# Kernel tuning notes

Measured on AMD Instinct MI355X. Metric: run time of the kernel, lower is better.

## Reference

```python
import jax, jax.numpy as jnp
import numpy as np

B, L, E, H = 2, 2048, 512, 8
D = E // H  # head_dim = 64


def setup_inputs() -> dict:
    key = jax.random.key(0)
    ks = jax.random.split(key, 12)
    s = 0.02
    return {
        "values": jax.random.normal(ks[0], (B, L, E), jnp.float32),
        "keys": jax.random.normal(ks[1], (B, L, E), jnp.float32),
        "query": jax.random.normal(ks[2], (B, L, E), jnp.float32),
        "mask": jax.random.randint(ks[3], (B, 1, L, L), 0, 2, jnp.int32),
        "Wv": jax.random.normal(ks[4], (E, E), jnp.float32) * s,
        "bv": jax.random.normal(ks[5], (E,), jnp.float32) * s,
        "Wk": jax.random.normal(ks[6], (E, E), jnp.float32) * s,
        "bk": jax.random.normal(ks[7], (E,), jnp.float32) * s,
        "Wq": jax.random.normal(ks[8], (E, E), jnp.float32) * s,
        "bq": jax.random.normal(ks[9], (E,), jnp.float32) * s,
        "Wo": jax.random.normal(ks[10], (E, E), jnp.float32) * s,
        "bo": jax.random.normal(ks[11], (E,), jnp.float32) * s,
    }


def reference(values, keys, query, mask, Wv, bv, Wk, bk, Wq, bq, Wo, bo):
    b, lq = query.shape[0], query.shape[1]
    # torch Linear: y = x @ W.T + b
    v = (values @ Wv.T + bv).reshape(b, -1, H, D)
    k = (keys @ Wk.T + bk).reshape(b, -1, H, D)
    q = (query @ Wq.T + bq).reshape(b, lq, H, D)
    energy = jnp.einsum("bqhd,bkhd->bhqk", q, k)  # [B,H,Lq,Lk]
    # mask applied BEFORE the scale, as in the original
    energy = jnp.where(mask == 0, jnp.float32(-1e20), energy)
    # NOTE: scales by sqrt(embed_size), not sqrt(head_dim) (faithful)
    attn = jax.nn.softmax(energy / jnp.sqrt(jnp.float32(E)), axis=3)
    out = jnp.einsum("bhql,blhd->bqhd", attn, v).reshape(b, lq, E)
    return out @ Wo.T + bo
```

## Files before the change

kernel.cpp:

```cpp
#include <hip/hip_runtime.h>
#include <hip/hip_bf16.h>
#include <math.h>

#define BB 2
#define LL 2048
#define EE 512
#define HH 8
#define DD 64
#define MM (BB * LL)
#define LW (LL / 64)

typedef short bf16x8 __attribute__((ext_vector_type(8)));
typedef float f32x4 __attribute__((ext_vector_type(4)));

#define MFMA16(a, b, c) __builtin_amdgcn_mfma_f32_16x16x32_bf16((a), (b), (c), 0, 0, 0)

__device__ __forceinline__ uint4 cvt8_bf16(const float4 a, const float4 b) {
    union { __hip_bfloat16 h[8]; uint4 u; } t;
    t.h[0] = __float2bfloat16(a.x); t.h[1] = __float2bfloat16(a.y);
    t.h[2] = __float2bfloat16(a.z); t.h[3] = __float2bfloat16(a.w);
    t.h[4] = __float2bfloat16(b.x); t.h[5] = __float2bfloat16(b.y);
    t.h[6] = __float2bfloat16(b.z); t.h[7] = __float2bfloat16(b.w);
    return t.u;
}

struct PrepArgs {
    const float* xsrc[3];
    __hip_bfloat16* xdst[3];
    const float* wsrc[4];
    __hip_bfloat16* wdst[4];
    const int* mask;
    unsigned long long* mbits;
};

__global__ __launch_bounds__(256) void prep(PrepArgs a) {
    const int blk = blockIdx.x;
    if (blk < 3072) {
        const int t = blk >> 10;
        const int i = ((blk & 1023) * 256 + threadIdx.x) * 8;
        const float* s = a.xsrc[t] + i;
        float4 f0 = *(const float4*)(s);
        float4 f1 = *(const float4*)(s + 4);
        *(uint4*)(a.xdst[t] + i) = cvt8_bf16(f0, f1);
    } else if (blk < 3584) {
        const int r = blk - 3072;
        const int t = r >> 7;
        const int i = ((r & 127) * 256 + threadIdx.x) * 8;
        const float* s = a.wsrc[t] + i;
        float4 f0 = *(const float4*)(s);
        float4 f1 = *(const float4*)(s + 4);
        *(uint4*)(a.wdst[t] + i) = cvt8_bf16(f0, f1);
    } else {
        const size_t idx = (size_t)(blk - 3584) * 256 + threadIdx.x;
        const int m = a.mask[idx];
        const unsigned long long w = __ballot(m != 0);
        if ((threadIdx.x & 63) == 0) a.mbits[idx >> 6] = w;
    }
}

__global__ __launch_bounds__(256) void transpose_v(
    const __hip_bfloat16* __restrict__ vb, __hip_bfloat16* __restrict__ vt) {
    __shared__ __hip_bfloat16 T[64][72];
    const int tid = threadIdx.x;
    const int l0 = blockIdx.x * 64;
    const int h = blockIdx.y;
    const int b = blockIdx.z;
    const int row = tid >> 2;
    const int cg = (tid & 3) * 16;

    const __hip_bfloat16* src = vb + ((size_t)b * LL + l0 + row) * EE + h * DD + cg;
    *(uint4*)&T[row][cg] = *(const uint4*)src;
    *(uint4*)&T[row][cg + 8] = *(const uint4*)(src + 8);
    __syncthreads();

    __hip_bfloat16 t[16];
    #pragma unroll
    for (int e = 0; e < 16; ++e) t[e] = T[cg + e][row];
    __hip_bfloat16* dst = vt + (((size_t)b * HH + h) * DD + row) * LL + l0 + cg;
    *(uint4*)&dst[0] = *(uint4*)&t[0];
    *(uint4*)&dst[8] = *(uint4*)&t[8];
}

struct QKVArgs {
    const __hip_bfloat16* X[3];
    const __hip_bfloat16* W[3];
    const float* bias[3];
    __hip_bfloat16* O[3];
};

__global__ __launch_bounds__(256) void gemm_qkv(QKVArgs p) {
    __shared__ __hip_bfloat16 Xs[128][72];
    __shared__ __hip_bfloat16 Ws[64][72];

    const int z = blockIdx.z;
    const __hip_bfloat16* __restrict__ X = p.X[z];
    const __hip_bfloat16* __restrict__ W = p.W[z];
    const float* __restrict__ bias = p.bias[z];
    __hip_bfloat16* __restrict__ O = p.O[z];
    const float oscale = (z == 0) ? 0.04419417382415922f : 1.0f;

    const int tid = threadIdx.x;
    const int wave = tid >> 6, lane = tid & 63;
    const int l15 = lane & 15, quad = lane >> 4;
    const int wm = wave * 32;
    const int m0 = blockIdx.y * 128, n0 = blockIdx.x * 64;

    const int arow = tid >> 1, acg = (tid & 1) * 32;
    const int brow = tid >> 2, bcg = (tid & 3) * 16;

    const __hip_bfloat16* Ag = X + (size_t)(m0 + arow) * EE + acg;
    const __hip_bfloat16* Bg = W + (size_t)(n0 + brow) * EE + bcg;

    f32x4 acc[2][4] = {};

    uint4 a0 = *(const uint4*)(Ag + 0),  a1 = *(const uint4*)(Ag + 8);
    uint4 a2 = *(const uint4*)(Ag + 16), a3 = *(const uint4*)(Ag + 24);
    uint4 b0 = *(const uint4*)(Bg + 0),  b1 = *(const uint4*)(Bg + 8);

    for (int k0 = 0; k0 < EE; k0 += 64) {
        *(uint4*)&Xs[arow][acg + 0]  = a0;
        *(uint4*)&Xs[arow][acg + 8]  = a1;
        *(uint4*)&Xs[arow][acg + 16] = a2;
        *(uint4*)&Xs[arow][acg + 24] = a3;
        *(uint4*)&Ws[brow][bcg + 0] = b0;
        *(uint4*)&Ws[brow][bcg + 8] = b1;
        __syncthreads();

        if (k0 + 64 < EE) {
            const __hip_bfloat16* an = Ag + k0 + 64;
            const __hip_bfloat16* bn = Bg + k0 + 64;
            a0 = *(const uint4*)(an + 0);  a1 = *(const uint4*)(an + 8);
            a2 = *(const uint4*)(an + 16); a3 = *(const uint4*)(an + 24);
            b0 = *(const uint4*)(bn + 0);  b1 = *(const uint4*)(bn + 8);
        }

        #pragma unroll
        for (int c = 0; c < 2; ++c) {
            bf16x8 af[2], bfr[4];
            #pragma unroll
            for (int i = 0; i < 2; ++i)
                af[i] = *(const bf16x8*)&Xs[wm + i * 16 + l15][c * 32 + quad * 8];
            #pragma unroll
            for (int j = 0; j < 4; ++j)
                bfr[j] = *(const bf16x8*)&Ws[j * 16 + l15][c * 32 + quad * 8];
            #pragma unroll
            for (int i = 0; i < 2; ++i)
                #pragma unroll
                for (int j = 0; j < 4; ++j)
                    acc[i][j] = MFMA16(af[i], bfr[j], acc[i][j]);
        }
        __syncthreads();
    }

    #pragma unroll
    for (int i = 0; i < 2; ++i)
        #pragma unroll
        for (int j = 0; j < 4; ++j) {
            const int n = n0 + j * 16 + l15;
            const float bv = bias[n];
            #pragma unroll
            for (int reg = 0; reg < 4; ++reg) {
                const int m = m0 + wm + i * 16 + quad * 4 + reg;
                O[(size_t)m * EE + n] = __float2bfloat16((acc[i][j][reg] + bv) * oscale);
            }
        }
}

__global__ __launch_bounds__(256) void gemm_out(
    const __hip_bfloat16* __restrict__ X, const __hip_bfloat16* __restrict__ W,
    const float* __restrict__ bias, float* __restrict__ C) {
    __shared__ __hip_bfloat16 Xs[128][72];
    __shared__ __hip_bfloat16 Ws[64][72];

    const int tid = threadIdx.x;
    const int wave = tid >> 6, lane = tid & 63;
    const int l15 = lane & 15, quad = lane >> 4;
    const int wm = wave * 32;
    const int m0 = blockIdx.y * 128, n0 = blockIdx.x * 64;

    const int arow = tid >> 1, acg = (tid & 1) * 32;
    const int brow = tid >> 2, bcg = (tid & 3) * 16;

    const __hip_bfloat16* Ag = X + (size_t)(m0 + arow) * EE + acg;
    const __hip_bfloat16* Bg = W + (size_t)(n0 + brow) * EE + bcg;

    f32x4 acc[2][4] = {};

    uint4 a0 = *(const uint4*)(Ag + 0),  a1 = *(const uint4*)(Ag + 8);
    uint4 a2 = *(const uint4*)(Ag + 16), a3 = *(const uint4*)(Ag + 24);
    uint4 b0 = *(const uint4*)(Bg + 0),  b1 = *(const uint4*)(Bg + 8);

    for (int k0 = 0; k0 < EE; k0 += 64) {
        *(uint4*)&Xs[arow][acg + 0]  = a0;
        *(uint4*)&Xs[arow][acg + 8]  = a1;
        *(uint4*)&Xs[arow][acg + 16] = a2;
        *(uint4*)&Xs[arow][acg + 24] = a3;
        *(uint4*)&Ws[brow][bcg + 0] = b0;
        *(uint4*)&Ws[brow][bcg + 8] = b1;
        __syncthreads();

        if (k0 + 64 < EE) {
            const __hip_bfloat16* an = Ag + k0 + 64;
            const __hip_bfloat16* bn = Bg + k0 + 64;
            a0 = *(const uint4*)(an + 0);  a1 = *(const uint4*)(an + 8);
            a2 = *(const uint4*)(an + 16); a3 = *(const uint4*)(an + 24);
            b0 = *(const uint4*)(bn + 0);  b1 = *(const uint4*)(bn + 8);
        }

        #pragma unroll
        for (int c = 0; c < 2; ++c) {
            bf16x8 af[2], bfr[4];
            #pragma unroll
            for (int i = 0; i < 2; ++i)
                af[i] = *(const bf16x8*)&Xs[wm + i * 16 + l15][c * 32 + quad * 8];
            #pragma unroll
            for (int j = 0; j < 4; ++j)
                bfr[j] = *(const bf16x8*)&Ws[j * 16 + l15][c * 32 + quad * 8];
            #pragma unroll
            for (int i = 0; i < 2; ++i)
                #pragma unroll
                for (int j = 0; j < 4; ++j)
                    acc[i][j] = MFMA16(af[i], bfr[j], acc[i][j]);
        }
        __syncthreads();
    }

    #pragma unroll
    for (int i = 0; i < 2; ++i)
        #pragma unroll
        for (int j = 0; j < 4; ++j) {
            const int n = n0 + j * 16 + l15;
            const float bv = bias[n];
            #pragma unroll
            for (int reg = 0; reg < 4; ++reg) {
                const int m = m0 + wm + i * 16 + quad * 4 + reg;
                C[(size_t)m * EE + n] = acc[i][j][reg] + bv;
            }
        }
}

__global__ __launch_bounds__(256) void attn_mfma(
    const __hip_bfloat16* __restrict__ Qb, const __hip_bfloat16* __restrict__ Kb,
    const __hip_bfloat16* __restrict__ vtg, const unsigned long long* __restrict__ mbits,
    __hip_bfloat16* __restrict__ Op) {
    __shared__ __hip_bfloat16 Ks[64][72];
    __shared__ __hip_bfloat16 Vs[64][72];
    __shared__ __hip_bfloat16 Ps[4][16][72];

    const int tid = threadIdx.x;
    const int wave = tid >> 6;
    const int lane = tid & 63;
    const int l15 = lane & 15;
    const int quad = lane >> 4;
    const int b = blockIdx.z;
    const int h = blockIdx.y;
    const int q0 = blockIdx.x * 64;

    const int srow = tid >> 2;
    const int scg = (tid & 3) * 16;
    const int myq = q0 + wave * 16 + l15;

    bf16x8 qf[2];
    {
        const __hip_bfloat16* qrow = Qb + ((size_t)b * LL + myq) * EE + h * DD;
        qf[0] = *(const bf16x8*)(qrow + quad * 8);
        qf[1] = *(const bf16x8*)(qrow + 32 + quad * 8);
    }

    const __hip_bfloat16* kbase = Kb + ((size_t)b * LL + srow) * EE + h * DD + scg;
    const __hip_bfloat16* vbase = vtg + (((size_t)b * HH + h) * DD + srow) * LL + scg;
    const unsigned long long* mrow = mbits + ((size_t)b * LL + myq) * LW;

    f32x4 o[4] = {};
    float lrun = 0.f;

    uint4 ka0 = *(const uint4*)(kbase);
    uint4 ka1 = *(const uint4*)(kbase + 8);
    uint4 va0 = *(const uint4*)(vbase);
    uint4 va1 = *(const uint4*)(vbase + 8);
    unsigned long long mw = mrow[0];

    for (int k0 = 0; k0 < LL; k0 += 64) {
        *(uint4*)&Ks[srow][scg] = ka0;
        *(uint4*)&Ks[srow][scg + 8] = ka1;
        *(uint4*)&Vs[srow][scg] = va0;
        *(uint4*)&Vs[srow][scg + 8] = va1;
        __syncthreads();

        unsigned long long mw_cur = mw;
        if (k0 + 64 < LL) {
            const __hip_bfloat16* kn = kbase + (size_t)(k0 + 64) * EE;
            const __hip_bfloat16* vn = vbase + k0 + 64;
            ka0 = *(const uint4*)(kn);
            ka1 = *(const uint4*)(kn + 8);
            va0 = *(const uint4*)(vn);
            va1 = *(const uint4*)(vn + 8);
            mw = mrow[(k0 >> 6) + 1];
        }

        f32x4 st[4] = {};
        #pragma unroll
        for (int mt = 0; mt < 4; ++mt) {
            bf16x8 a0 = *(const bf16x8*)&Ks[mt * 16 + l15][quad * 8];
            bf16x8 a1 = *(const bf16x8*)&Ks[mt * 16 + l15][32 + quad * 8];
            st[mt] = MFMA16(a0, qf[0], st[mt]);
            st[mt] = MFMA16(a1, qf[1], st[mt]);
        }

        #pragma unroll
        for (int mt = 0; mt < 4; ++mt) {
            float p[4];
            #pragma unroll
            for (int reg = 0; reg < 4; ++reg) {
                const bool live = (mw_cur >> (mt * 16 + quad * 4 + reg)) & 1ull;
                p[reg] = __expf(live ? st[mt][reg] : -1e30f);
                lrun += p[reg];
            }
            union { __hip_bfloat16 h[4]; ushort4 v; } pk;
            pk.h[0] = __float2bfloat16(p[0]);
            pk.h[1] = __float2bfloat16(p[1]);
            pk.h[2] = __float2bfloat16(p[2]);
            pk.h[3] = __float2bfloat16(p[3]);
            *(ushort4*)&Ps[wave][l15][mt * 16 + quad * 4] = pk.v;
        }

        bf16x8 pa0 = *(const bf16x8*)&Ps[wave][l15][quad * 8];
        bf16x8 pa1 = *(const bf16x8*)&Ps[wave][l15][32 + quad * 8];
        #pragma unroll
        for (int nt = 0; nt < 4; ++nt) {
            bf16x8 vb0 = *(const bf16x8*)&Vs[nt * 16 + l15][quad * 8];
            bf16x8 vb1 = *(const bf16x8*)&Vs[nt * 16 + l15][32 + quad * 8];
            o[nt] = MFMA16(pa0, vb0, o[nt]);
            o[nt] = MFMA16(pa1, vb1, o[nt]);
        }
        __syncthreads();
    }

    lrun += __shfl_xor(lrun, 16);
    lrun += __shfl_xor(lrun, 32);
    const float linv = 1.f / lrun;
    float linvR[4];
    #pragma unroll
    for (int reg = 0; reg < 4; ++reg)
        linvR[reg] = __shfl(linv, quad * 4 + reg);

    __hip_bfloat16* Ob = Op + ((size_t)b * LL + q0 + wave * 16) * EE + h * DD;
    #pragma unroll
    for (int nt = 0; nt < 4; ++nt)
        #pragma unroll
        for (int reg = 0; reg < 4; ++reg) {
            const int qrow = quad * 4 + reg;
            Ob[(size_t)qrow * EE + nt * 16 + l15] =
                __float2bfloat16(o[nt][reg] * linvR[reg]);
        }
}

extern "C" void kernel_launch(void* const* d_in, const int* in_sizes, int n_in,
                              void* d_out, int out_size, void* d_ws, size_t ws_size,
                              hipStream_t stream) {
    const float* values = (const float*)d_in[0];
    const float* keys   = (const float*)d_in[1];
    const float* query  = (const float*)d_in[2];
    const int*   mask   = (const int*)d_in[3];
    const float* Wv = (const float*)d_in[4];
    const float* bv = (const float*)d_in[5];
    const float* Wk = (const float*)d_in[6];
    const float* bk = (const float*)d_in[7];
    const float* Wq = (const float*)d_in[8];
    const float* bq = (const float*)d_in[9];
    const float* Wo = (const float*)d_in[10];
    const float* bo = (const float*)d_in[11];
    float* out = (float*)d_out;

    const size_t XS = (size_t)MM * EE * 2;
    const size_t WS = (size_t)EE * EE * 2;
    char* w = (char*)d_ws;
    __hip_bfloat16* xq  = (__hip_bfloat16*)(w);
    __hip_bfloat16* xk  = (__hip_bfloat16*)(w + XS);
    __hip_bfloat16* xv  = (__hip_bfloat16*)(w + 2 * XS);
    __hip_bfloat16* qb  = (__hip_bfloat16*)(w + 3 * XS);
    __hip_bfloat16* kb  = (__hip_bfloat16*)(w + 4 * XS);
    __hip_bfloat16* vb  = (__hip_bfloat16*)(w + 5 * XS);
    __hip_bfloat16* vtg = (__hip_bfloat16*)(w + 6 * XS);
    __hip_bfloat16* aob = (__hip_bfloat16*)(w + 7 * XS);
    __hip_bfloat16* wqb = (__hip_bfloat16*)(w + 8 * XS);
    __hip_bfloat16* wkb = (__hip_bfloat16*)(w + 8 * XS + WS);
    __hip_bfloat16* wvb = (__hip_bfloat16*)(w + 8 * XS + 2 * WS);
    __hip_bfloat16* wob = (__hip_bfloat16*)(w + 8 * XS + 3 * WS);
    unsigned long long* mbits = (unsigned long long*)(w + 8 * XS + 4 * WS);

    PrepArgs pa;
    pa.xsrc[0] = query; pa.xsrc[1] = keys; pa.xsrc[2] = values;
    pa.xdst[0] = xq;    pa.xdst[1] = xk;   pa.xdst[2] = xv;
    pa.wsrc[0] = Wq; pa.wsrc[1] = Wk; pa.wsrc[2] = Wv; pa.wsrc[3] = Wo;
    pa.wdst[0] = wqb; pa.wdst[1] = wkb; pa.wdst[2] = wvb; pa.wdst[3] = wob;
    pa.mask = mask; pa.mbits = mbits;

    QKVArgs qa;
    qa.X[0] = xq;  qa.X[1] = xk;  qa.X[2] = xv;
    qa.W[0] = wqb; qa.W[1] = wkb; qa.W[2] = wvb;
    qa.bias[0] = bq; qa.bias[1] = bk; qa.bias[2] = bv;
    qa.O[0] = qb;  qa.O[1] = kb;  qa.O[2] = vb;

    prep<<<36352, 256, 0, stream>>>(pa);
    gemm_qkv<<<dim3(EE / 64, MM / 128, 3), 256, 0, stream>>>(qa);
    transpose_v<<<dim3(LL / 64, HH, BB), 256, 0, stream>>>(vb, vtg);
    attn_mfma<<<dim3(LL / 64, HH, BB), 256, 0, stream>>>(qb, kb, vtg, mbits, aob);
    gemm_out<<<dim3(EE / 64, MM / 128), 256, 0, stream>>>(aob, wob, bo, out);
}
```

Measured before the change: 188.7 us.

## Use 128x128 GEMM tiles with direct global-to-LDS loads and double-buffer attention K/V

The QKV and output projection GEMMs move from 128x64 to 128x128 tiles with a 4x4 MFMA accumulator per wave. They fill shared memory with global_load_lds (K step 32, no padding) instead of staging through registers. The attention kernel double-buffers K/V tiles in shared memory so the next tile's stores overlap with compute, and it computes the exp unconditionally and zeroes masked entries with split row-sum accumulators. Risks include fewer GEMM blocks (lower occupancy on a large GPU), possible LDS bank conflicts from the unpadded layout, no software prefetch in the GEMMs, and more LDS use in attention.

```diff
diff --git a/kernel.cpp b/kernel.cpp
--- a/kernel.cpp
+++ b/kernel.cpp
@@ -14,6 +14,13 @@
 typedef float f32x4 __attribute__((ext_vector_type(4)));
 
 #define MFMA16(a, b, c) __builtin_amdgcn_mfma_f32_16x16x32_bf16((a), (b), (c), 0, 0, 0)
+
+__device__ __forceinline__ void gl2lds16(const __hip_bfloat16* g, __hip_bfloat16* l) {
+    __builtin_amdgcn_global_load_lds(
+        (const __attribute__((address_space(1))) unsigned int*)(g),
+        (__attribute__((address_space(3))) unsigned int*)(l),
+        16, 0, 0);
+}
 
 __device__ __forceinline__ uint4 cvt8_bf16(const float4 a, const float4 b) {
     union { __hip_bfloat16 h[8]; uint4 u; } t;
@@ -88,9 +95,9 @@
     __hip_bfloat16* O[3];
 };
 
-__global__ __launch_bounds__(256) void gemm_qkv(QKVArgs p) {
-    __shared__ __hip_bfloat16 Xs[128][72];
-    __shared__ __hip_bfloat16 Ws[64][72];
+__global__ __launch_bounds__(256) void gemm_qkv128(QKVArgs p) {
+    __shared__ __hip_bfloat16 As[128 * 32];
+    __shared__ __hip_bfloat16 Bs[128 * 32];
 
     const int z = blockIdx.z;
     const __hip_bfloat16* __restrict__ X = p.X[z];
@@ -102,61 +109,45 @@
     const int tid = threadIdx.x;
     const int wave = tid >> 6, lane = tid & 63;
     const int l15 = lane & 15, quad = lane >> 4;
-    const int wm = wave * 32;
-    const int m0 = blockIdx.y * 128, n0 = blockIdx.x * 64;
-
-    const int arow = tid >> 1, acg = (tid & 1) * 32;
-    const int brow = tid >> 2, bcg = (tid & 3) * 16;
-
-    const __hip_bfloat16* Ag = X + (size_t)(m0 + arow) * EE + acg;
-    const __hip_bfloat16* Bg = W + (size_t)(n0 + brow) * EE + bcg;
-
-    f32x4 acc[2][4] = {};
-
-    uint4 a0 = *(const uint4*)(Ag + 0),  a1 = *(const uint4*)(Ag + 8);
-    uint4 a2 = *(const uint4*)(Ag + 16), a3 = *(const uint4*)(Ag + 24);
-    uint4 b0 = *(const uint4*)(Bg + 0),  b1 = *(const uint4*)(Bg + 8);
-
-    for (int k0 = 0; k0 < EE; k0 += 64) {
-        *(uint4*)&Xs[arow][acg + 0]  = a0;
-        *(uint4*)&Xs[arow][acg + 8]  = a1;
-        *(uint4*)&Xs[arow][acg + 16] = a2;
-        *(uint4*)&Xs[arow][acg + 24] = a3;
-        *(uint4*)&Ws[brow][bcg + 0] = b0;
-        *(uint4*)&Ws[brow][bcg + 8] = b1;
+    const int wm = (wave >> 1) * 64, wn = (wave & 1) * 64;
+    const int m0 = blockIdx.y * 128, n0 = blockIdx.x * 128;
+
+    const int srow = wave * 32 + (lane >> 2);
+    const int scol = (lane & 3) * 8;
+    const __hip_bfloat16* Ag = X + (size_t)(m0 + srow) * EE + scol;
+    const __hip_bfloat16* Bg = W + (size_t)(n0 + srow) * EE + scol;
+    __hip_bfloat16* Al = As + wave * 32 * 32;
+    __hip_bfloat16* Bl = Bs + wave * 32 * 32;
+
+    f32x4 acc[4][4] = {};
+
+    for (int k0 = 0; k0 < EE; k0 += 32) {
+        gl2lds16(Ag + k0, Al);
+        gl2lds16(Ag + k0 + (size_t)16 * EE, Al + 16 * 32);
+        gl2lds16(Bg + k0, Bl);
+        gl2lds16(Bg + k0 + (size_t)16 * EE, Bl + 16 * 32);
         __syncthreads();
 
-        if (k0 + 64 < EE) {
-            const __hip_bfloat16* an = Ag + k0 + 64;
-            const __hip_bfloat16* bn = Bg + k0 + 64;
-            a0 = *(const uint4*)(an + 0);  a1 = *(const uint4*)(an + 8);
-            a2 = *(const uint4*)(an + 16); a3 = *(const uint4*)(an + 24);
-            b0 = *(const uint4*)(bn + 0);  b1 = *(const uint4*)(bn + 8);
-        }
-
-        #pragma unroll
-        for (int c = 0; c < 2; ++c) {
-            bf16x8 af[2], bfr[4];
-            #pragma unroll
-            for (int i = 0; i < 2; ++i)
-                af[i] = *(const bf16x8*)&Xs[wm + i * 16 + l15][c * 32 + quad * 8];
+        bf16x8 af[4], bfr[4];
+        #pragma unroll
+        for (int i = 0; i < 4; ++i)
+            af[i] = *(const bf16x8*)&As[(wm + i * 16 + l15) * 32 + quad * 8];
+        #pragma unroll
+        for (int j = 0; j < 4; ++j)
+            bfr[j] = *(const bf16x8*)&Bs[(wn + j * 16 + l15) * 32 + quad * 8];
+        #pragma unroll
+        for (int i = 0; i < 4; ++i)
             #pragma unroll
             for (int j = 0; j < 4; ++j)
-                bfr[j] = *(const bf16x8*)&Ws[j * 16 + l15][c * 32 + quad * 8];
-            #pragma unroll
-            for (int i = 0; i < 2; ++i)
-                #pragma unroll
-                for (int j = 0; j < 4; ++j)
-                    acc[i][j] = MFMA16(af[i], bfr[j], acc[i][j]);
-        }
+                acc[i][j] = MFMA16(af[i], bfr[j], acc[i][j]);
         __syncthreads();
     }
 
     #pragma unroll
-    for (int i = 0; i < 2; ++i)
+    for (int i = 0; i < 4; ++i)
         #pragma unroll
         for (int j = 0; j < 4; ++j) {
-            const int n = n0 + j * 16 + l15;
+            const int n = n0 + wn + j * 16 + l15;
             const float bv = bias[n];
             #pragma unroll
             for (int reg = 0; reg < 4; ++reg) {
@@ -166,70 +157,54 @@
         }
 }
 
-__global__ __launch_bounds__(256) void gemm_out(
+__global__ __launch_bounds__(256) void gemm_out128(
     const __hip_bfloat16* __restrict__ X, const __hip_bfloat16* __restrict__ W,
     const float* __restrict__ bias, float* __restrict__ C) {
-    __shared__ __hip_bfloat16 Xs[128][72];
-    __shared__ __hip_bfloat16 Ws[64][72];
+    __shared__ __hip_bfloat16 As[128 * 32];
+    __shared__ __hip_bfloat16 Bs[128 * 32];
 
     const int tid = threadIdx.x;
     const int wave = tid >> 6, lane = tid & 63;
     const int l15 = lane & 15, quad = lane >> 4;
-    const int wm = wave * 32;
-    const int m0 = blockIdx.y * 128, n0 = blockIdx.x * 64;
-
-    const int arow = tid >> 1, acg = (tid & 1) * 32;
-    const int brow = tid >> 2, bcg = (tid & 3) * 16;
-
-    const __hip_bfloat16* Ag = X + (size_t)(m0 + arow) * EE + acg;
-    const __hip_bfloat16* Bg = W + (size_t)(n0 + brow) * EE + bcg;
-
-    f32x4 acc[2][4] = {};
-
-    uint4 a0 = *(const uint4*)(Ag + 0),  a1 = *(const uint4*)(Ag + 8);
-    uint4 a2 = *(const uint4*)(Ag + 16), a3 = *(const uint4*)(Ag + 24);
-    uint4 b0 = *(const uint4*)(Bg + 0),  b1 = *(const uint4*)(Bg + 8);
-
-    for (int k0 = 0; k0 < EE; k0 += 64) {
-        *(uint4*)&Xs[arow][acg + 0]  = a0;
-        *(uint4*)&Xs[arow][acg + 8]  = a1;
-        *(uint4*)&Xs[arow][acg + 16] = a2;
-        *(uint4*)&Xs[arow][acg + 24] = a3;
-        *(uint4*)&Ws[brow][bcg + 0] = b0;
-        *(uint4*)&Ws[brow][bcg + 8] = b1;
+    const int wm = (wave >> 1) * 64, wn = (wave & 1) * 64;
+    const int m0 = blockIdx.y * 128, n0 = blockIdx.x * 128;
+
+    const int srow = wave * 32 + (lane >> 2);
+    const int scol = (lane & 3) * 8;
+    const __hip_bfloat16* Ag = X + (size_t)(m0 + srow) * EE + scol;
+    const __hip_bfloat16* Bg = W + (size_t)(n0 + srow) * EE + scol;
+    __hip_bfloat16* Al = As + wave * 32 * 32;
+    __hip_bfloat16* Bl = Bs + wave * 32 * 32;
+
+    f32x4 acc[4][4] = {};
+
+    for (int k0 = 0; k0 < EE; k0 += 32) {
+        gl2lds16(Ag + k0, Al);
+        gl2lds16(Ag + k0 + (size_t)16 * EE, Al + 16 * 32);
+        gl2lds16(Bg + k0, Bl);
+        gl2lds16(Bg + k0 + (size_t)16 * EE, Bl + 16 * 32);
         __syncthreads();
 
-        if (k0 + 64 < EE) {
-            const __hip_bfloat16* an = Ag + k0 + 64;
-            const __hip_bfloat16* bn = Bg + k0 + 64;
-            a0 = *(const uint4*)(an + 0);  a1 = *(const uint4*)(an + 8);
-            a2 = *(const uint4*)(an + 16); a3 = *(const uint4*)(an + 24);
-            b0 = *(const uint4*)(bn + 0);  b1 = *(const uint4*)(bn + 8);
-        }
-
-        #pragma unroll
-        for (int c = 0; c < 2; ++c) {
-            bf16x8 af[2], bfr[4];
-            #pragma unroll
-            for (int i = 0; i < 2; ++i)
-                af[i] = *(const bf16x8*)&Xs[wm + i * 16 + l15][c * 32 + quad * 8];
+        bf16x8 af[4], bfr[4];
+        #pragma unroll
+        for (int i = 0; i < 4; ++i)
+            af[i] = *(const bf16x8*)&As[(wm + i * 16 + l15) * 32 + quad * 8];
+        #pragma unroll
+        for (int j = 0; j < 4; ++j)
+            bfr[j] = *(const bf16x8*)&Bs[(wn + j * 16 + l15) * 32 + quad * 8];
+        #pragma unroll
+        for (int i = 0; i < 4; ++i)
             #pragma unroll
             for (int j = 0; j < 4; ++j)
-                bfr[j] = *(const bf16x8*)&Ws[j * 16 + l15][c * 32 + quad * 8];
-            #pragma unroll
-            for (int i = 0; i < 2; ++i)
-                #pragma unroll
-                for (int j = 0; j < 4; ++j)
-                    acc[i][j] = MFMA16(af[i], bfr[j], acc[i][j]);
-        }
+                acc[i][j] = MFMA16(af[i], bfr[j], acc[i][j]);
         __syncthreads();
     }
 
     #pragma unroll
-    for (int i = 0; i < 2; ++i)
+    for (int i = 0; i < 4; ++i)
         #pragma unroll
         for (int j = 0; j < 4; ++j) {
-            const int n = n0 + j * 16 + l15;
+            const int n = n0 + wn + j * 16 + l15;
             const float bv = bias[n];
             #pragma unroll
             for (int reg = 0; reg < 4; ++reg) {
@@ -243,8 +218,8 @@
     const __hip_bfloat16* __restrict__ Qb, const __hip_bfloat16* __restrict__ Kb,
     const __hip_bfloat16* __restrict__ vtg, const unsigned long long* __restrict__ mbits,
     __hip_bfloat16* __restrict__ Op) {
-    __shared__ __hip_bfloat16 Ks[64][72];
-    __shared__ __hip_bfloat16 Vs[64][72];
+    __shared__ __hip_bfloat16 Ks[2][64][72];
+    __shared__ __hip_bfloat16 Vs[2][64][72];
     __shared__ __hip_bfloat16 Ps[4][16][72];
 
     const int tid = threadIdx.x;
@@ -272,37 +247,43 @@
     const unsigned long long* mrow = mbits + ((size_t)b * LL + myq) * LW;
 
     f32x4 o[4] = {};
-    float lrun = 0.f;
-
-    uint4 ka0 = *(const uint4*)(kbase);
-    uint4 ka1 = *(const uint4*)(kbase + 8);
-    uint4 va0 = *(const uint4*)(vbase);
-    uint4 va1 = *(const uint4*)(vbase + 8);
-    unsigned long long mw = mrow[0];
-
-    for (int k0 = 0; k0 < LL; k0 += 64) {
-        *(uint4*)&Ks[srow][scg] = ka0;
-        *(uint4*)&Ks[srow][scg + 8] = ka1;
-        *(uint4*)&Vs[srow][scg] = va0;
-        *(uint4*)&Vs[srow][scg + 8] = va1;
-        __syncthreads();
-
-        unsigned long long mw_cur = mw;
-        if (k0 + 64 < LL) {
-            const __hip_bfloat16* kn = kbase + (size_t)(k0 + 64) * EE;
-            const __hip_bfloat16* vn = vbase + k0 + 64;
+    float lr0 = 0.f, lr1 = 0.f;
+
+    {
+        uint4 k0a = *(const uint4*)(kbase);
+        uint4 k0b = *(const uint4*)(kbase + 8);
+        uint4 v0a = *(const uint4*)(vbase);
+        uint4 v0b = *(const uint4*)(vbase + 8);
+        *(uint4*)&Ks[0][srow][scg] = k0a;
+        *(uint4*)&Ks[0][srow][scg + 8] = k0b;
+        *(uint4*)&Vs[0][srow][scg] = v0a;
+        *(uint4*)&Vs[0][srow][scg + 8] = v0b;
+    }
+    unsigned long long mw_cur = mrow[0];
+    __syncthreads();
+
+    for (int t = 0; t < LW; ++t) {
+        const int cur = t & 1;
+        const int nxt = cur ^ 1;
+        const bool more = (t + 1) < LW;
+
+        uint4 ka0, ka1, va0, va1;
+        unsigned long long mw_n;
+        if (more) {
+            const __hip_bfloat16* kn = kbase + (size_t)(t + 1) * 64 * EE;
+            const __hip_bfloat16* vn = vbase + (t + 1) * 64;
             ka0 = *(const uint4*)(kn);
             ka1 = *(const uint4*)(kn + 8);
             va0 = *(const uint4*)(vn);
             va1 = *(const uint4*)(vn + 8);
-            mw = mrow[(k0 >> 6) + 1];
+            mw_n = mrow[t + 1];
         }
 
         f32x4 st[4] = {};
         #pragma unroll
         for (int mt = 0; mt < 4; ++mt) {
-            bf16x8 a0 = *(const bf16x8*)&Ks[mt * 16 + l15][quad * 8];
-            bf16x8 a1 = *(const bf16x8*)&Ks[mt * 16 + l15][32 + quad * 8];
+            bf16x8 a0 = *(const bf16x8*)&Ks[cur][mt * 16 + l15][quad * 8];
+            bf16x8 a1 = *(const bf16x8*)&Ks[cur][mt * 16 + l15][32 + quad * 8];
             st[mt] = MFMA16(a0, qf[0], st[mt]);
             st[mt] = MFMA16(a1, qf[1], st[mt]);
         }
@@ -313,9 +294,11 @@
             #pragma unroll
             for (int reg = 0; reg < 4; ++reg) {
                 const bool live = (mw_cur >> (mt * 16 + quad * 4 + reg)) & 1ull;
-                p[reg] = __expf(live ? st[mt][reg] : -1e30f);
-                lrun += p[reg];
+                const float e = __expf(st[mt][reg]);
+                p[reg] = live ? e : 0.f;
             }
+            lr0 += p[0] + p[1];
+            lr1 += p[2] + p[3];
             union { __hip_bfloat16 h[4]; ushort4 v; } pk;
             pk.h[0] = __float2bfloat16(p[0]);
             pk.h[1] = __float2bfloat16(p[1]);
@@ -328,14 +311,23 @@
         bf16x8 pa1 = *(const bf16x8*)&Ps[wave][l15][32 + quad * 8];
         #pragma unroll
         for (int nt = 0; nt < 4; ++nt) {
-            bf16x8 vb0 = *(const bf16x8*)&Vs[nt * 16 + l15][quad * 8];
-            bf16x8 vb1 = *(const bf16x8*)&Vs[nt * 16 + l15][32 + quad * 8];
+            bf16x8 vb0 = *(const bf16x8*)&Vs[cur][nt * 16 + l15][quad * 8];
+            bf16x8 vb1 = *(const bf16x8*)&Vs[cur][nt * 16 + l15][32 + quad * 8];
             o[nt] = MFMA16(pa0, vb0, o[nt]);
             o[nt] = MFMA16(pa1, vb1, o[nt]);
         }
+
+        if (more) {
+            *(uint4*)&Ks[nxt][srow][scg] = ka0;
+            *(uint4*)&Ks[nxt][srow][scg + 8] = ka1;
+            *(uint4*)&Vs[nxt][srow][scg] = va0;
+            *(uint4*)&Vs[nxt][srow][scg + 8] = va1;
+            mw_cur = mw_n;
+        }
         __syncthreads();
     }
 
+    float lrun = lr0 + lr1;
     lrun += __shfl_xor(lrun, 16);
     lrun += __shfl_xor(lrun, 32);
     const float linv = 1.f / lrun;
@@ -403,8 +395,8 @@
     qa.O[0] = qb;  qa.O[1] = kb;  qa.O[2] = vb;
 
     prep<<<36352, 256, 0, stream>>>(pa);
-    gemm_qkv<<<dim3(EE / 64, MM / 128, 3), 256, 0, stream>>>(qa);
+    gemm_qkv128<<<dim3(EE / 128, MM / 128, 3), 256, 0, stream>>>(qa);
     transpose_v<<<dim3(LL / 64, HH, BB), 256, 0, stream>>>(vb, vtg);
     attn_mfma<<<dim3(LL / 64, HH, BB), 256, 0, stream>>>(qb, kb, vtg, mbits, aob);
-    gemm_out<<<dim3(EE / 64, MM / 128), 256, 0, stream>>>(aob, wob, bo, out);
-}
+    gemm_out128<<<dim3(EE / 128, MM / 128), 256, 0, stream>>>(aob, wob, bo, out);
+}
```

Result: no change. 189.8 us (+0.5%).
